# Kernel optimization log

Measured on AMD Instinct MI355X. Metric: run time of the kernel, lower is better.

Reference implementation:

```python
import jax, jax.numpy as jnp
import numpy as np

EMB = 512
HEADS = 8
HEAD_DIM = EMB // HEADS
GN_EPS = 1e-6
THETA_SCALE = 10000.0


def _multiply_by_i(x):
    # interleave: out[..., 2i] = -x[..., 2i+1], out[..., 2i+1] = x[..., 2i]
    return jnp.stack((-x[..., 1::2], x[..., ::2]), axis=-1).reshape(x.shape)


def _theta_shift(x, sin, cos):
    return x * cos + _multiply_by_i(x) * sin


def setup_inputs() -> dict:
    key = jax.random.key(0)
    ks = jax.random.split(key, 13)
    B, N, E = 2, 2048, EMB

    def xavier(k, out_dim, in_dim):
        std = (2.0 / (out_dim + in_dim)) ** 0.5
        return std * jax.random.normal(k, (out_dim, in_dim), dtype=jnp.float32)

    return {
        "query": jax.random.normal(ks[0], (B, N, E), dtype=jnp.float32),
        "k": jax.random.normal(ks[1], (B, N, E), dtype=jnp.float32),
        "v": jax.random.normal(ks[2], (B, N, E), dtype=jnp.float32),
        "Wq": xavier(ks[3], E, E), "bq": jnp.zeros((E,), jnp.float32),
        "Wk": xavier(ks[4], E, E), "bk": jnp.zeros((E,), jnp.float32),
        "Wv": xavier(ks[5], E, E), "bv": jnp.zeros((E,), jnp.float32),
        "Wg": xavier(ks[6], E, E), "bg": jnp.zeros((E,), jnp.float32),
        "Wo": xavier(ks[7], E, E), "bo": jnp.zeros((E,), jnp.float32),
    }


def reference(query, k, v, Wq, bq, Wk, bk, Wv, bv, Wg, bg, Wo, bo):
    B, N, E = query.shape
    H, D = HEADS, E // HEADS

    def proj(x, W, b):  # torch Linear: x @ W.T + b, then split heads -> [b h n d]
        return (x @ W.T + b).reshape(B, N, H, D).transpose(0, 2, 1, 3)

    q = proj(query, Wq, bq)
    kk = proj(k, Wk, bk)
    vv = proj(v, Wv, bv)

    # rotary-style theta shift; thetas repeated pairwise [t0,t0,t1,t1,...]
    thetas = jnp.repeat(1.0 / THETA_SCALE ** jnp.linspace(0.0, 1.0, D // 2), 2)
    angles = jnp.arange(N, dtype=jnp.float32)[:, None] * thetas[None, :]  # [n d]
    sin = jnp.sin(angles)[None, None]
    cos = jnp.cos(angles)[None, None]
    q = _theta_shift(q, sin, cos)
    kk = _theta_shift(kk, sin, cos)

    # decay-masked retention (softmax-free)
    gammas = 1.0 - jnp.exp(jnp.linspace(np.log(1 / 32), np.log(1 / 512), H)).astype(jnp.float32)
    pos = jnp.arange(N)
    dist = jnp.abs(pos[:, None] - pos[None, :]).astype(jnp.float32)
    causal = pos[:, None] >= pos[None, :]
    decay_mask = jnp.where(causal[None], gammas[:, None, None] ** dist[None], 0.0)  # [h n s]

    kk = kk / (D ** 0.5)
    sim = jnp.einsum('bhnd,bhsd->bhns', q, kk) * decay_mask[None]  # [b h n n]
    ret = jnp.einsum('bhns,bhsd->bhnd', sim, vv)

    # GroupNorm(groups=H, channels=H, affine=False) over (b n) samples -> per-(b,h,n) norm over d
    mean = ret.mean(axis=-1, keepdims=True)
    var = ret.var(axis=-1, keepdims=True)
    ret = (ret - mean) / jnp.sqrt(var + GN_EPS)

    ret = ret.transpose(0, 2, 1, 3).reshape(B, N, E)
    gate = jax.nn.silu(query @ Wg.T + bg)
    out = (ret * gate) @ Wo.T + bo
    return out
```

## Files before the change

### kernel.cpp

```cpp
#include <hip/hip_runtime.h>
#include <math.h>

typedef float f32x4 __attribute__((ext_vector_type(4)));
typedef short s16x8 __attribute__((ext_vector_type(8)));
typedef short s16x4 __attribute__((ext_vector_type(4)));
typedef unsigned u32x4 __attribute__((ext_vector_type(4)));

__device__ __forceinline__ short f2bf(float f) {
    unsigned u = __builtin_bit_cast(unsigned, f);
    unsigned r = u + 0x7FFFu + ((u >> 16) & 1u);
    return (short)(r >> 16);
}
__device__ __forceinline__ float bf2f(short h) {
    return __builtin_bit_cast(float, ((unsigned)(unsigned short)h) << 16);
}
__device__ __forceinline__ unsigned pack2(short a, short b) {
    return (unsigned)(unsigned short)a | ((unsigned)(unsigned short)b << 16);
}
__device__ __forceinline__ unsigned cvtpk(float a, float b) {
    unsigned r;
    asm("v_cvt_pk_bf16_f32 %0, %1, %2" : "=v"(r) : "v"(a), "v"(b));
    return r;
}

__device__ __forceinline__ void split16v(const float* __restrict__ p,
                                         short* __restrict__ h,
                                         short* __restrict__ l) {
    f32x4 a0 = *(const f32x4*)(p);
    f32x4 a1 = *(const f32x4*)(p + 4);
    f32x4 a2 = *(const f32x4*)(p + 8);
    f32x4 a3 = *(const f32x4*)(p + 12);
    #pragma unroll
    for (int i = 0; i < 4; ++i) {
        short t0;
        t0 = f2bf(a0[i]); h[i]      = t0; l[i]      = f2bf(a0[i] - bf2f(t0));
        t0 = f2bf(a1[i]); h[4 + i]  = t0; l[4 + i]  = f2bf(a1[i] - bf2f(t0));
        t0 = f2bf(a2[i]); h[8 + i]  = t0; l[8 + i]  = f2bf(a2[i] - bf2f(t0));
        t0 = f2bf(a3[i]); h[12 + i] = t0; l[12 + i] = f2bf(a3[i] - bf2f(t0));
    }
}

__device__ __forceinline__ void gload16(const void* g, void* l) {
    __builtin_amdgcn_global_load_lds(
        (const __attribute__((address_space(1))) unsigned int*)g,
        (__attribute__((address_space(3))) unsigned int*)l,
        16, 0, 0);
}

__device__ __forceinline__ void decay_params(int h, int n0, float& l2g, int& stLo) {
    float lg0 = logf(1.0f / 32.0f), lg1 = logf(1.0f / 512.0f);
    float om = expf(lg0 + (float)h * (lg1 - lg0) * (1.0f / 7.0f));
    l2g = log2f(1.0f - om);
    int Dcut = (int)(11.5129255f / om) + 64;
    stLo = (n0 - Dcut) >> 6;
    if (stLo < 0) stLo = 0;
}

__global__ __launch_bounds__(256) void presplit_kernel(
    const float* __restrict__ W0, const float* __restrict__ W1,
    const float* __restrict__ W2, const float* __restrict__ W3,
    const float* __restrict__ W4,
    short* __restrict__ Wsp, float2* __restrict__ SC)
{
    const int blk = blockIdx.x;
    const int t = threadIdx.x;
    short hbuf[16], lbuf[16];
    if (blk < 256) {
        const int w = blk >> 6, bi = blk & 63;
        const float* src = (w == 0) ? W0 : (w == 1) ? W1 : (w == 2) ? W2 : W3;
        const int idx = (bi * 256 + t) * 16;
        const int row = idx >> 9, k0 = idx & 511;
        const int ntile = row >> 7, r = row & 127;
        const int kstep = k0 >> 5, kk0 = k0 & 31;
        const int s = (r & 3) << 4;
        split16v(src + idx, hbuf, lbuf);
        short* hp = Wsp + (long)w * 524288 + (ntile * 16 + kstep) * 8192 + r * 32;
        short* lp = hp + 4096;
        const int oA = ((2 * kk0) ^ s) >> 1;
        const int oB = ((2 * kk0 + 16) ^ s) >> 1;
        *(s16x8*)(hp + oA) = *(s16x8*)(hbuf);
        *(s16x8*)(hp + oB) = *(s16x8*)(hbuf + 8);
        *(s16x8*)(lp + oA) = *(s16x8*)(lbuf);
        *(s16x8*)(lp + oB) = *(s16x8*)(lbuf + 8);
    } else if (blk < 320) {
        const int bi = blk - 256;
        const int idx = (bi * 256 + t) * 16;
        short* hi = Wsp + (long)4 * 524288;
        short* lo = hi + 262144;
        split16v(W4 + idx, hbuf, lbuf);
        *(s16x8*)(hi + idx)     = *(s16x8*)(hbuf);
        *(s16x8*)(hi + idx + 8) = *(s16x8*)(hbuf + 8);
        *(s16x8*)(lo + idx)     = *(s16x8*)(lbuf);
        *(s16x8*)(lo + idx + 8) = *(s16x8*)(lbuf + 8);
    } else {
        const int gid = (blk - 320) * 256 + t;
        const int pos = gid >> 5, pp = gid & 31;
        const float theta = powf(10000.0f, -(float)pp * (1.0f / 31.0f));
        const float ang = (float)pos * theta;
        SC[gid] = make_float2(cosf(ang), sinf(ang));
    }
}

__global__ __launch_bounds__(512, 4) void projqkvg_kernel(
    const float* __restrict__ X0, const float* __restrict__ X1,
    const float* __restrict__ X2, const short* __restrict__ Wsp,
    const float* __restrict__ bq, const float* __restrict__ bk,
    const float* __restrict__ bv, const float* __restrict__ bg,
    const float2* __restrict__ SC,
    short* __restrict__ Qh, short* __restrict__ Ql,
    short* __restrict__ Kh, short* __restrict__ Vth,
    float* __restrict__ G)
{
    __shared__ __align__(16) short SB[36864];

    const int fid = blockIdx.x + 4 * (blockIdx.y + 64 * blockIdx.z);
    const int mtile = fid & 63;
    const int rr = fid >> 6;
    const int mode = rr & 3;
    const int ntile = rr >> 2;
    const int m0 = mtile * 64, n0 = ntile * 128;

    const int xi = (mode == 1) ? 1 : (mode == 2) ? 2 : 0;
    const float* Xf = (xi == 0) ? X0 : (xi == 1) ? X1 : X2;
    const float* bias = (mode == 0) ? bq : (mode == 1) ? bk
                       : (mode == 2) ? bv : bg;

    const int t = threadIdx.x, lane = t & 63, wv = t >> 6;
    const int wm = wv >> 1, wn = wv & 1;
    const int quad = lane >> 4, l15 = lane & 15;

    const short* Wblk = Wsp + (long)mode * 524288 + (long)ntile * 16 * 8192;

    const int c0 = wv * 3;
    const char* gs[3];
    int gstp[3];
    #pragma unroll
    for (int i = 0; i < 3; ++i) {
        const int c = c0 + i;
        if (c < 8) {
            const int u = c * 64 + lane;
            const int row = u >> 3, ucol = u & 7;
            gs[i] = (const char*)(Xf + (long)(m0 + row) * 512)
                    + ((ucol ^ (row & 7)) << 4);
            gstp[i] = 128;
        } else {
            gs[i] = (const char*)(Wblk + (c - 8) * 512 + lane * 8);
            gstp[i] = 16384;
        }
    }

    auto STAGE = [&](int stg, int ks) {
        char* dstb = (char*)SB + stg * 24576 + c0 * 1024;
        #pragma unroll
        for (int i = 0; i < 3; ++i)
            gload16(gs[i] + (long)ks * gstp[i], dstb + i * 1024);
    };

    int aoff;
    {
        const int row = wm * 16 + l15;
        aoff = row * 128 + ((quad * 32) ^ ((row & 7) << 4));
    }
    const int sxw = (l15 & 3) << 4;
    int boff[4];
    #pragma unroll
    for (int s2 = 0; s2 < 4; ++s2)
        boff[s2] = 8192 + (wn * 64 + s2 * 16 + l15) * 64 + ((quad * 16) ^ sxw);

    f32x4 acc[4];
    #pragma unroll
    for (int j = 0; j < 4; ++j)
        acc[j] = (f32x4){0.f, 0.f, 0.f, 0.f};

    STAGE(0, 0);
    STAGE(1, 1);
    asm volatile("s_waitcnt vmcnt(3)" ::: "memory");
    __builtin_amdgcn_s_barrier();

    int cur = 0;
    for (int ks = 0; ks < 16; ++ks) {
        if (ks < 14) {
            int fill = cur + 2; if (fill >= 3) fill -= 3;
            STAGE(fill, ks + 2);
        }
        __builtin_amdgcn_sched_barrier(0);

        const char* stg = (const char*)SB + cur * 24576;
        s16x8 ah, al, bh[4], bl[4];
        {
            f32x4 x0 = *(const f32x4*)(stg + aoff);
            f32x4 x1 = *(const f32x4*)(stg + (aoff ^ 16));
            u32x4 hv, lv;
            #pragma unroll
            for (int j = 0; j < 2; ++j) {
                float a0 = x0[2 * j], b0 = x0[2 * j + 1];
                float a1 = x1[2 * j], b1 = x1[2 * j + 1];
                unsigned h0 = cvtpk(a0, b0);
                unsigned h1 = cvtpk(a1, b1);
                hv[j]     = h0;
                hv[2 + j] = h1;
                float fa0 = __builtin_bit_cast(float, h0 << 16);
                float fb0 = __builtin_bit_cast(float, h0 & 0xFFFF0000u);
                float fa1 = __builtin_bit_cast(float, h1 << 16);
                float fb1 = __builtin_bit_cast(float, h1 & 0xFFFF0000u);
                lv[j]     = cvtpk(a0 - fa0, b0 - fb0);
                lv[2 + j] = cvtpk(a1 - fa1, b1 - fb1);
            }
            ah = __builtin_bit_cast(s16x8, hv);
            al = __builtin_bit_cast(s16x8, lv);
        }
        #pragma unroll
        for (int s2 = 0; s2 < 4; ++s2) {
            bh[s2] = *(const s16x8*)(stg + boff[s2]);
            bl[s2] = *(const s16x8*)(stg + 8192 + boff[s2]);
        }
        __builtin_amdgcn_s_setprio(1);
        #pragma unroll
        for (int j = 0; j < 4; ++j) {
            acc[j] = __builtin_amdgcn_mfma_f32_16x16x32_bf16(ah, bh[j], acc[j], 0, 0, 0);
            acc[j] = __builtin_amdgcn_mfma_f32_16x16x32_bf16(al, bh[j], acc[j], 0, 0, 0);
            acc[j] = __builtin_amdgcn_mfma_f32_16x16x32_bf16(ah, bl[j], acc[j], 0, 0, 0);
        }
        __builtin_amdgcn_s_setprio(0);

        if (ks < 14)       asm volatile("s_waitcnt vmcnt(3)" ::: "memory");
        else if (ks == 14) asm volatile("s_waitcnt vmcnt(0)" ::: "memory");
        __builtin_amdgcn_sched_barrier(0);
        __builtin_amdgcn_s_barrier();

        cur += 1; if (cur >= 3) cur -= 3;
    }

    __syncthreads();

    const int bb = m0 >> 11, posb = m0 & 2047;
    const int head = (n0 >> 6) + wn;

    if (mode == 0) {
        short* Thi = SB + wv * 2304;
        short* Tlo = Thi + 1152;
        #pragma unroll
        for (int ns = 0; ns < 4; ++ns) {
            const int col = n0 + wn * 64 + ns * 16 + l15;
            const float bvv = bias[col];
            const int pp = (ns * 16 + l15) >> 1;
            #pragma unroll
            for (int r = 0; r < 4; ++r) {
                const int m = m0 + wm * 16 + quad * 4 + r;
                const int pos = m & 2047;
                float x = acc[ns][r] + bvv;
                float prt = __shfl_xor(x, 1);
                float2 sc = SC[pos * 32 + pp];
                float y0 = x * sc.x - prt * sc.y;
                float y1 = prt * sc.x + x * sc.y;
                if (!(l15 & 1)) {
                    short h0 = f2bf(y0), h1 = f2bf(y1);
                    short l0 = f2bf(y0 - bf2f(h0)), l1 = f2bf(y1 - bf2f(h1));
                    const int o = (quad * 4 + r) * 72 + ns * 16 + l15;
                    *(unsigned*)&Thi[o] = pack2(h0, h1);
                    *(unsigned*)&Tlo[o] = pack2(l0, l1);
                }
            }
        }
        #pragma unroll
        for (int p2 = 0; p2 < 2; ++p2) {
            const int row = p2 * 8 + (lane >> 3);
            const int ch = (lane & 7) * 8;
            s16x8 vh = *(const s16x8*)&Thi[row * 72 + ch];
            s16x8 vl = *(const s16x8*)&Tlo[row * 72 + ch];
            const long o = ((long)(bb * 8 + head) * 2048 + posb + wm * 16 + row) * 64 + ch;
            *(s16x8*)(Qh + o) = vh;
            *(s16x8*)(Ql + o) = vl;
        }
    } else if (mode == 1) {
        short* Thi = SB + wv * 1152;
        #pragma unroll
        for (int ns = 0; ns < 4; ++ns) {
            const int col = n0 + wn * 64 + ns * 16 + l15;
            const float bvv = bias[col];
            const int pp = (ns * 16 + l15) >> 1;
            #pragma unroll
            for (int r = 0; r < 4; ++r) {
                const int m = m0 + wm * 16 + quad * 4 + r;
                const int pos = m & 2047;
                float x = acc[ns][r] + bvv;
                float prt = __shfl_xor(x, 1);
                float2 sc = SC[pos * 32 + pp];
                float y0 = (x * sc.x - prt * sc.y) * 0.125f;
                float y1 = (prt * sc.x + x * sc.y) * 0.125f;
                if (!(l15 & 1)) {
                    const int o = (quad * 4 + r) * 72 + ns * 16 + l15;
                    *(unsigned*)&Thi[o] = pack2(f2bf(y0), f2bf(y1));
                }
            }
        }
        #pragma unroll
        for (int p2 = 0; p2 < 2; ++p2) {
            const int row = p2 * 8 + (lane >> 3);
            const int ch = (lane & 7) * 8;
            s16x8 vh = *(const s16x8*)&Thi[row * 72 + ch];
            const long o = ((long)(bb * 8 + head) * 2048 + posb + wm * 16 + row) * 64 + ch;
            *(s16x8*)(Kh + o) = vh;
        }
    } else if (mode == 2) {
        short* T2 = SB;
        #pragma unroll
        for (int ns = 0; ns < 4; ++ns) {
            const int col = n0 + wn * 64 + ns * 16 + l15;
            const float bvv = bias[col];
            s16x4 pk;
            #pragma unroll
            for (int r = 0; r < 4; ++r)
                pk[r] = f2bf(acc[ns][r] + bvv);
            *(s16x4*)&T2[(wn * 64 + ns * 16 + l15) * 72
                         + wm * 16 + quad * 4] = pk;
        }
        __syncthreads();
        #pragma unroll
        for (int pass = 0; pass < 2; ++pass) {
            const int row = pass * 64 + (t >> 3);
            const int ch = (t & 7) * 8;
            s16x8 v = *(const s16x8*)&T2[row * 72 + ch];
            const int hd = (n0 >> 6) + (row >> 6);
            const int d = row & 63;
            const long o = ((long)(bb * 8 + hd) * 64 + d) * 2048 + posb + ch;
            *(s16x8*)(Vth + o) = v;
        }
    } else {
        #pragma unroll
        for (int ns = 0; ns < 4; ++ns) {
            const int col = n0 + wn * 64 + ns * 16 + l15;
            const float bvv = bias[col];
            #pragma unroll
            for (int r = 0; r < 4; ++r) {
                const int m = m0 + wm * 16 + quad * 4 + r;
                float x = acc[ns][r] + bvv;
                G[(long)m * 512 + col] = x / (1.0f + expf(-x));
            }
        }
    }
}

__global__ __launch_bounds__(256) void attn_chunk_kernel(
    const short* __restrict__ Qh_g, const short* __restrict__ Ql_g,
    const short* __restrict__ Kh_g, const short* __restrict__ Vth_g,
    const float* __restrict__ G, short* __restrict__ RGh,
    float* __restrict__ Racc)
{
    __shared__ __align__(16) short KhS[2][4608], VhS[2][4608];
    __shared__ __align__(16) short PhS[4352];

    const int fid = blockIdx.x;
    const int bh = fid & 15;
    const int rest = fid >> 4;
    const int qt = rest & 31;
    const int c  = rest >> 5;
    const int h = bh & 7, b = bh >> 3;
    const int n0 = qt * 64;

    float l2g;
    int stLo;
    decay_params(h, n0, l2g, stLo);
    const int ntiles = qt - stLo + 1;
    const int st0 = stLo + c * 16;
    if (st0 > qt) return;
    const int stHi = min(st0 + 15, qt);

    const int t = threadIdx.x, lane = t & 63, wv = t >> 6;
    const int quad = lane >> 4, l15 = lane & 15;
    const long base = (long)bh * 2048 * 64;

    float gneg[16];
    #pragma unroll
    for (int i = 0; i < 16; ++i)
        gneg[i] = exp2f(-(float)((i >> 2) * 16 + (i & 3)) * l2g);

    const int srow = t >> 2;
    const int scol = (t & 3) * 16;
    const int n = n0 + wv * 16 + l15;

    s16x8 qh[2], ql[2];
    {
        const short* qp  = Qh_g + base + (long)(n0 + wv * 16 + l15) * 64 + quad * 8;
        const short* qp2 = Ql_g + base + (long)(n0 + wv * 16 + l15) * 64 + quad * 8;
        qh[0] = *(const s16x8*)qp;
        qh[1] = *(const s16x8*)(qp + 32);
        ql[0] = *(const s16x8*)qp2;
        ql[1] = *(const s16x8*)(qp2 + 32);
    }

    f32x4 racc[4];
    #pragma unroll
    for (int i = 0; i < 4; ++i) racc[i] = (f32x4){0.f, 0.f, 0.f, 0.f};

    s16x8 pk0, pk1, pv0, pv1;
    {
        const long ko = base + (long)(st0 * 64 + srow) * 64 + scol;
        pk0 = *(const s16x8*)(Kh_g + ko);
        pk1 = *(const s16x8*)(Kh_g + ko + 8);
        const long vo = base + (long)srow * 2048 + st0 * 64 + scol;
        pv0 = *(const s16x8*)(Vth_g + vo);
        pv1 = *(const s16x8*)(Vth_g + vo + 8);
    }
    *(s16x8*)&KhS[0][srow * 72 + scol]     = pk0;
    *(s16x8*)&KhS[0][srow * 72 + scol + 8] = pk1;
    *(s16x8*)&VhS[0][srow * 72 + scol]     = pv0;
    *(s16x8*)&VhS[0][srow * 72 + scol + 8] = pv1;
    __syncthreads();

    int cur = 0;
    for (int st = st0; st <= stHi; ++st, cur ^= 1) {
        if (st < stHi) {
            const long ko = base + (long)((st + 1) * 64 + srow) * 64 + scol;
            pk0 = *(const s16x8*)(Kh_g + ko);
            pk1 = *(const s16x8*)(Kh_g + ko + 8);
            const long vo = base + (long)srow * 2048 + (st + 1) * 64 + scol;
            pv0 = *(const s16x8*)(Vth_g + vo);
            pv1 = *(const s16x8*)(Vth_g + vo + 8);
        }

        const short* khs = KhS[cur];
        const short* vhs = VhS[cur];
        const int s0 = st * 64;
        const float t0 = exp2f((float)(n - s0 - quad * 4) * l2g);

        #pragma unroll
        for (int sub = 0; sub < 4; ++sub) {
            const int ro = (sub * 16 + l15) * 72 + quad * 8;
            s16x8 kh0 = *(const s16x8*)&khs[ro];
            s16x8 kh1 = *(const s16x8*)&khs[ro + 32];
            f32x4 sacc = (f32x4){0.f, 0.f, 0.f, 0.f};
            __builtin_amdgcn_s_setprio(1);
            sacc = __builtin_amdgcn_mfma_f32_16x16x32_bf16(kh0, qh[0], sacc, 0, 0, 0);
            sacc = __builtin_amdgcn_mfma_f32_16x16x32_bf16(kh1, qh[1], sacc, 0, 0, 0);
            sacc = __builtin_amdgcn_mfma_f32_16x16x32_bf16(kh0, ql[0], sacc, 0, 0, 0);
            sacc = __builtin_amdgcn_mfma_f32_16x16x32_bf16(kh1, ql[1], sacc, 0, 0, 0);
            __builtin_amdgcn_s_setprio(0);

            const int sb = s0 + sub * 16 + quad * 4;
            s16x4 pkh;
            #pragma unroll
            for (int r = 0; r < 4; ++r) {
                const int s = sb + r;
                const float wgt = (n >= s) ? t0 * gneg[sub * 4 + r] : 0.0f;
                pkh[r] = f2bf(sacc[r] * wgt);
            }
            *(s16x4*)&PhS[(wv * 16 + l15) * 68 + sub * 16 + quad * 4] = pkh;
        }

        const int pro = (wv * 16 + l15) * 68 + quad * 8;
        s16x8 ph0 = *(const s16x8*)&PhS[pro];
        s16x8 ph1 = *(const s16x8*)&PhS[pro + 32];
        __builtin_amdgcn_s_setprio(1);
        #pragma unroll
        for (int ds = 0; ds < 4; ++ds) {
            const int ro = (ds * 16 + l15) * 72 + quad * 8;
            s16x8 vh0 = *(const s16x8*)&vhs[ro];
            s16x8 vh1 = *(const s16x8*)&vhs[ro + 32];
            racc[ds] = __builtin_amdgcn_mfma_f32_16x16x32_bf16(ph0, vh0, racc[ds], 0, 0, 0);
            racc[ds] = __builtin_amdgcn_mfma_f32_16x16x32_bf16(ph1, vh1, racc[ds], 0, 0, 0);
        }
        __builtin_amdgcn_s_setprio(0);

        if (st < stHi) {
            short* kd = KhS[cur ^ 1];
            short* vd = VhS[cur ^ 1];
            *(s16x8*)&kd[srow * 72 + scol]     = pk0;
            *(s16x8*)&kd[srow * 72 + scol + 8] = pk1;
            *(s16x8*)&vd[srow * 72 + scol]     = pv0;
            *(s16x8*)&vd[srow * 72 + scol + 8] = pv1;
        }
        __syncthreads();
    }

    if (c == 0 && ntiles <= 16) {
        float mean[4], rstd[4];
        #pragma unroll
        for (int r = 0; r < 4; ++r) {
            float s = racc[0][r] + racc[1][r] + racc[2][r] + racc[3][r];
            s += __shfl_xor(s, 1); s += __shfl_xor(s, 2);
            s += __shfl_xor(s, 4); s += __shfl_xor(s, 8);
            mean[r] = s * (1.0f / 64.0f);
            float vs = 0.f;
            #pragma unroll
            for (int ds = 0; ds < 4; ++ds) {
                float d = racc[ds][r] - mean[r];
                vs += d * d;
            }
            vs += __shfl_xor(vs, 1); vs += __shfl_xor(vs, 2);
            vs += __shfl_xor(vs, 4); vs += __shfl_xor(vs, 8);
            rstd[r] = rsqrtf(vs * (1.0f / 64.0f) + 1e-6f);
        }
        short* rgH = (short*)KhS + wv * 1152;
        #pragma unroll
        for (int ds = 0; ds < 4; ++ds) {
            #pragma unroll
            for (int r = 0; r < 4; ++r) {
                const int nn = n0 + wv * 16 + quad * 4 + r;
                const int d = ds * 16 + l15;
                const long gi = ((long)(b * 2048 + nn)) * 512 + h * 64 + d;
                float rg = (racc[ds][r] - mean[r]) * rstd[r] * G[gi];
                float prt = __shfl_xor(rg, 1);
                if (!(l15 & 1)) {
                    const int o = (quad * 4 + r) * 72 + ds * 16 + l15;
                    *(unsigned*)&rgH[o] = pack2(f2bf(rg), f2bf(prt));
                }
            }
        }
        #pragma unroll
        for (int p2 = 0; p2 < 2; ++p2) {
            const int row = p2 * 8 + (lane >> 3);
            const int ch = (lane & 7) * 8;
            s16x8 vh = *(const s16x8*)&rgH[row * 72 + ch];
            const int nn = n0 + wv * 16 + row;
            const long o = ((long)(b * 2048 + nn)) * 512 + h * 64 + ch;
            *(s16x8*)(RGh + o) = vh;
        }
        return;
    }

    float* dst = Racc + (long)((bh * 32 + qt) * 2 + c) * 4096;
    #pragma unroll
    for (int ds = 0; ds < 4; ++ds)
        #pragma unroll
        for (int r = 0; r < 4; ++r)
            dst[(wv * 16 + quad * 4 + r) * 64 + ds * 16 + l15] = racc[ds][r];
}

__global__ __launch_bounds__(256) void attn_finish_kernel(
    const float* __restrict__ Racc, const float* __restrict__ G,
    short* __restrict__ RGh)
{
    __shared__ __align__(16) short rgS[4608];

    const int fid = blockIdx.x;
    const int bh = fid & 15;
    const int qt = fid >> 4;
    const int h = bh & 7, b = bh >> 3;
    const int n0 = qt * 64;

    float l2g;
    int stLo;
    decay_params(h, n0, l2g, stLo);
    const int ntiles = qt - stLo + 1;
    if (ntiles <= 16) return;

    const int t = threadIdx.x, lane = t & 63, wv = t >> 6;
    const int quad = lane >> 4, l15 = lane & 15;

    const float* s0 = Racc + (long)((bh * 32 + qt) * 2) * 4096;
    f32x4 racc[4];
    #pragma unroll
    for (int ds = 0; ds < 4; ++ds)
        #pragma unroll
        for (int r = 0; r < 4; ++r) {
            const int o = (wv * 16 + quad * 4 + r) * 64 + ds * 16 + l15;
            racc[ds][r] = s0[o] + s0[4096 + o];
        }

    float mean[4], rstd[4];
    #pragma unroll
    for (int r = 0; r < 4; ++r) {
        float s = racc[0][r] + racc[1][r] + racc[2][r] + racc[3][r];
        s += __shfl_xor(s, 1); s += __shfl_xor(s, 2);
        s += __shfl_xor(s, 4); s += __shfl_xor(s, 8);
        mean[r] = s * (1.0f / 64.0f);
        float vs = 0.f;
        #pragma unroll
        for (int ds = 0; ds < 4; ++ds) {
            float d = racc[ds][r] - mean[r];
            vs += d * d;
        }
        vs += __shfl_xor(vs, 1); vs += __shfl_xor(vs, 2);
        vs += __shfl_xor(vs, 4); vs += __shfl_xor(vs, 8);
        rstd[r] = rsqrtf(vs * (1.0f / 64.0f) + 1e-6f);
    }

    short* rgH = rgS + wv * 1152;
    #pragma unroll
    for (int ds = 0; ds < 4; ++ds) {
        #pragma unroll
        for (int r = 0; r < 4; ++r) {
            const int nn = n0 + wv * 16 + quad * 4 + r;
            const int d = ds * 16 + l15;
            const long gi = ((long)(b * 2048 + nn)) * 512 + h * 64 + d;
            float rg = (racc[ds][r] - mean[r]) * rstd[r] * G[gi];
            float prt = __shfl_xor(rg, 1);
            if (!(l15 & 1)) {
                const int o = (quad * 4 + r) * 72 + ds * 16 + l15;
                *(unsigned*)&rgH[o] = pack2(f2bf(rg), f2bf(prt));
            }
        }
    }
    __syncthreads();
    #pragma unroll
    for (int p2 = 0; p2 < 2; ++p2) {
        const int row = p2 * 8 + (lane >> 3);
        const int ch = (lane & 7) * 8;
        s16x8 vh = *(const s16x8*)&rgS[(wv * 1152 + row * 72 + ch)];
        const int nn = n0 + wv * 16 + row;
        const long o = ((long)(b * 2048 + nn)) * 512 + h * 64 + ch;
        *(s16x8*)(RGh + o) = vh;
    }
}

__global__ __launch_bounds__(256) void projo_kernel(
    const short* __restrict__ RGh, const short* __restrict__ Woh_g,
    const float* __restrict__ bo, float* __restrict__ out)
{
    __shared__ __align__(16) char PB[46080];

    const short* Wol_g = Woh_g + 262144;
    const int t = threadIdx.x, lane = t & 63, wv = t >> 6;
    const int wm = wv >> 1, wn = wv & 1;
    const int quad = lane >> 4, l15 = lane & 15;
    const int m0 = blockIdx.y * 32, n0 = blockIdx.x * 128;

    f32x4 acc[4];
    #pragma unroll
    for (int j = 0; j < 4; ++j) acc[j] = (f32x4){0.f, 0.f, 0.f, 0.f};

    const int xrow = t >> 3, xcol = (t & 7) * 4;
    const int wrow = t >> 1, wcol = (t & 1) * 16;
    const long xbase = (long)(m0 + xrow) * 512 + xcol;
    const long wbase = (long)(n0 + wrow) * 512 + wcol;

    s16x4 px;
    s16x8 pw0, pw1, pw2, pw3;
    px  = *(const s16x4*)(RGh + xbase);
    pw0 = *(const s16x8*)(Woh_g + wbase);
    pw1 = *(const s16x8*)(Woh_g + wbase + 8);
    pw2 = *(const s16x8*)(Wol_g + wbase);
    pw3 = *(const s16x8*)(Wol_g + wbase + 8);

    {
        short* XhS = (short*)PB;
        short* WhS = XhS + 1280;
        short* WlS = XhS + 6400;
        *(s16x4*)&XhS[xrow * 40 + xcol]     = px;
        *(s16x8*)&WhS[wrow * 40 + wcol]     = pw0;
        *(s16x8*)&WhS[wrow * 40 + wcol + 8] = pw1;
        *(s16x8*)&WlS[wrow * 40 + wcol]     = pw2;
        *(s16x8*)&WlS[wrow * 40 + wcol + 8] = pw3;
    }
    __syncthreads();

    for (int k0 = 0; k0 < 512; k0 += 32) {
        const int cur = (k0 >> 5) & 1;
        const bool more = (k0 + 32 < 512);
        if (more) {
            const long xo = xbase + k0 + 32;
            const long wo = wbase + k0 + 32;
            px  = *(const s16x4*)(RGh + xo);
            pw0 = *(const s16x8*)(Woh_g + wo);
            pw1 = *(const s16x8*)(Woh_g + wo + 8);
            pw2 = *(const s16x8*)(Wol_g + wo);
            pw3 = *(const s16x8*)(Wol_g + wo + 8);
        }

        const short* XhS = (const short*)(PB + cur * 23040);
        const short* WhS = XhS + 1280;
        const short* WlS = XhS + 6400;
        s16x8 ah, bh[4], bl[4];
        {
            const int ro = (wm * 16 + l15) * 40 + quad * 8;
            ah = *(const s16x8*)&XhS[ro];
        }
        #pragma unroll
        for (int s = 0; s < 4; ++s) {
            const int ro = (wn * 64 + s * 16 + l15) * 40 + quad * 8;
            bh[s] = *(const s16x8*)&WhS[ro];
            bl[s] = *(const s16x8*)&WlS[ro];
        }
        #pragma unroll
        for (int j = 0; j < 4; ++j) {
            acc[j] = __builtin_amdgcn_mfma_f32_16x16x32_bf16(ah, bh[j], acc[j], 0, 0, 0);
            acc[j] = __builtin_amdgcn_mfma_f32_16x16x32_bf16(ah, bl[j], acc[j], 0, 0, 0);
        }

        if (more) {
            short* XhD = (short*)(PB + (cur ^ 1) * 23040);
            short* WhD = XhD + 1280;
            short* WlD = XhD + 6400;
            *(s16x4*)&XhD[xrow * 40 + xcol]     = px;
            *(s16x8*)&WhD[wrow * 40 + wcol]     = pw0;
            *(s16x8*)&WhD[wrow * 40 + wcol + 8] = pw1;
            *(s16x8*)&WlD[wrow * 40 + wcol]     = pw2;
            *(s16x8*)&WlD[wrow * 40 + wcol + 8] = pw3;
        }
        __syncthreads();
    }

    float* T = (float*)PB + wv * 1152;
    #pragma unroll
    for (int ns = 0; ns < 4; ++ns) {
        const int col = n0 + wn * 64 + ns * 16 + l15;
        const float bvv = bo[col];
        #pragma unroll
        for (int r = 0; r < 4; ++r)
            T[(quad * 4 + r) * 72 + ns * 16 + l15] = acc[ns][r] + bvv;
    }
    #pragma unroll
    for (int it = 0; it < 2; ++it) {
        const int row = it * 8 + (lane >> 3);
        const int ch = (lane & 7) * 8;
        f32x4 a = *(const f32x4*)&T[row * 72 + ch];
        f32x4 c = *(const f32x4*)&T[row * 72 + ch + 4];
        const long o = (long)(m0 + wm * 16 + row) * 512 + n0 + wn * 64 + ch;
        *(f32x4*)(out + o) = a;
        *(f32x4*)(out + o + 4) = c;
    }
}

extern "C" void kernel_launch(void* const* d_in, const int* in_sizes, int n_in,
                              void* d_out, int out_size, void* d_ws, size_t ws_size,
                              hipStream_t stream) {
    const float* query = (const float*)d_in[0];
    const float* kin   = (const float*)d_in[1];
    const float* vin   = (const float*)d_in[2];
    const float* Wq = (const float*)d_in[3];
    const float* bq = (const float*)d_in[4];
    const float* Wk = (const float*)d_in[5];
    const float* bk = (const float*)d_in[6];
    const float* Wv = (const float*)d_in[7];
    const float* bv = (const float*)d_in[8];
    const float* Wg = (const float*)d_in[9];
    const float* bg = (const float*)d_in[10];
    const float* Wo = (const float*)d_in[11];
    const float* bo = (const float*)d_in[12];

    short* S = (short*)d_ws;
    const long NE = 2097152;
    short* WSp = S;
    short* Xsp = S + 2621440;
    short* Qh  = Xsp + 12582912;
    short* Ql  = Qh + NE;
    short* Kh  = Ql + NE;
    short* Vth = Kh + NE;
    float* G   = (float*)(Vth + NE);
    short* RGh = (short*)(G + NE);
    float2* SC = (float2*)(RGh + NE);
    float* Racc = (float*)Xsp;

    presplit_kernel<<<576, 256, 0, stream>>>(
        Wq, Wk, Wv, Wg, Wo, WSp, SC);
    projqkvg_kernel<<<dim3(4, 64, 4), 512, 0, stream>>>(
        query, kin, vin, WSp, bq, bk, bv, bg, SC, Qh, Ql, Kh, Vth, G);
    attn_chunk_kernel<<<1024, 256, 0, stream>>>(
        Qh, Ql, Kh, Vth, G, RGh, Racc);
    attn_finish_kernel<<<512, 256, 0, stream>>>(
        Racc, G, RGh);
    projo_kernel<<<dim3(4, 128), 256, 0, stream>>>(
        RGh, WSp + 4 * 524288, bo, (float*)d_out);
}
```

Measured before the change: 181.5 us.

## Load projection activations directly into registers instead of staging through LDS

The projection kernel no longer stages the fp32 activation tile through shared memory. Each lane now loads its own A fragment straight from global memory into registers, prefetched two k-steps ahead, and only the split-bf16 weights stay in the 3-stage LDS pipeline. This cuts LDS use per block, so launch bounds rise to 6 blocks per SM for more occupancy. The trade-off is uncoalesced, redundant global reads of X across waves that share rows, plus more live registers and a vmcnt accounting that must stay correct.

```diff
diff --git a/kernel.cpp b/kernel.cpp
--- a/kernel.cpp
+++ b/kernel.cpp
@@ -101,7 +101,7 @@
     }
 }
 
-__global__ __launch_bounds__(512, 4) void projqkvg_kernel(
+__global__ __launch_bounds__(512, 6) void projqkvg_kernel(
     const float* __restrict__ X0, const float* __restrict__ X1,
     const float* __restrict__ X2, const short* __restrict__ Wsp,
     const float* __restrict__ bq, const float* __restrict__ bk,
@@ -111,7 +111,7 @@
     short* __restrict__ Kh, short* __restrict__ Vth,
     float* __restrict__ G)
 {
-    __shared__ __align__(16) short SB[36864];
+    __shared__ __align__(16) short SB[24576];
 
     const int fid = blockIdx.x + 4 * (blockIdx.y + 64 * blockIdx.z);
     const int mtile = fid & 63;
@@ -131,70 +131,60 @@
 
     const short* Wblk = Wsp + (long)mode * 524288 + (long)ntile * 16 * 8192;
 
-    const int c0 = wv * 3;
-    const char* gs[3];
-    int gstp[3];
-    #pragma unroll
-    for (int i = 0; i < 3; ++i) {
-        const int c = c0 + i;
-        if (c < 8) {
-            const int u = c * 64 + lane;
-            const int row = u >> 3, ucol = u & 7;
-            gs[i] = (const char*)(Xf + (long)(m0 + row) * 512)
-                    + ((ucol ^ (row & 7)) << 4);
-            gstp[i] = 128;
-        } else {
-            gs[i] = (const char*)(Wblk + (c - 8) * 512 + lane * 8);
-            gstp[i] = 16384;
-        }
-    }
+    const int c0 = wv * 2;
+    const char* gs[2];
+    #pragma unroll
+    for (int i = 0; i < 2; ++i)
+        gs[i] = (const char*)(Wblk + (c0 + i) * 512 + lane * 8);
 
     auto STAGE = [&](int stg, int ks) {
-        char* dstb = (char*)SB + stg * 24576 + c0 * 1024;
-        #pragma unroll
-        for (int i = 0; i < 3; ++i)
-            gload16(gs[i] + (long)ks * gstp[i], dstb + i * 1024);
+        char* dstb = (char*)SB + stg * 16384 + c0 * 1024;
+        #pragma unroll
+        for (int i = 0; i < 2; ++i)
+            gload16(gs[i] + (long)ks * 16384, dstb + i * 1024);
     };
 
-    int aoff;
-    {
-        const int row = wm * 16 + l15;
-        aoff = row * 128 + ((quad * 32) ^ ((row & 7) << 4));
-    }
+    const float* xp = Xf + (long)(m0 + wm * 16 + l15) * 512 + quad * 8;
+
     const int sxw = (l15 & 3) << 4;
     int boff[4];
     #pragma unroll
     for (int s2 = 0; s2 < 4; ++s2)
-        boff[s2] = 8192 + (wn * 64 + s2 * 16 + l15) * 64 + ((quad * 16) ^ sxw);
+        boff[s2] = (wn * 64 + s2 * 16 + l15) * 64 + ((quad * 16) ^ sxw);
 
     f32x4 acc[4];
     #pragma unroll
     for (int j = 0; j < 4; ++j)
         acc[j] = (f32x4){0.f, 0.f, 0.f, 0.f};
 
+    f32x4 x0c = *(const f32x4*)(xp);
+    f32x4 x1c = *(const f32x4*)(xp + 4);
+    f32x4 x0n = *(const f32x4*)(xp + 32);
+    f32x4 x1n = *(const f32x4*)(xp + 36);
     STAGE(0, 0);
     STAGE(1, 1);
-    asm volatile("s_waitcnt vmcnt(3)" ::: "memory");
+    asm volatile("s_waitcnt vmcnt(2)" ::: "memory");
     __builtin_amdgcn_s_barrier();
 
     int cur = 0;
     for (int ks = 0; ks < 16; ++ks) {
+        f32x4 x0f = x0c, x1f = x1c;
         if (ks < 14) {
+            x0f = *(const f32x4*)(xp + (ks + 2) * 32);
+            x1f = *(const f32x4*)(xp + (ks + 2) * 32 + 4);
             int fill = cur + 2; if (fill >= 3) fill -= 3;
             STAGE(fill, ks + 2);
         }
         __builtin_amdgcn_sched_barrier(0);
 
-        const char* stg = (const char*)SB + cur * 24576;
+        const char* stg = (const char*)SB + cur * 16384;
         s16x8 ah, al, bh[4], bl[4];
         {
-            f32x4 x0 = *(const f32x4*)(stg + aoff);
-            f32x4 x1 = *(const f32x4*)(stg + (aoff ^ 16));
             u32x4 hv, lv;
             #pragma unroll
             for (int j = 0; j < 2; ++j) {
-                float a0 = x0[2 * j], b0 = x0[2 * j + 1];
-                float a1 = x1[2 * j], b1 = x1[2 * j + 1];
+                float a0 = x0c[2 * j], b0 = x0c[2 * j + 1];
+                float a1 = x1c[2 * j], b1 = x1c[2 * j + 1];
                 unsigned h0 = cvtpk(a0, b0);
                 unsigned h1 = cvtpk(a1, b1);
                 hv[j]     = h0;
@@ -223,11 +213,12 @@
         }
         __builtin_amdgcn_s_setprio(0);
 
-        if (ks < 14)       asm volatile("s_waitcnt vmcnt(3)" ::: "memory");
+        if (ks < 14)       asm volatile("s_waitcnt vmcnt(4)" ::: "memory");
         else if (ks == 14) asm volatile("s_waitcnt vmcnt(0)" ::: "memory");
         __builtin_amdgcn_sched_barrier(0);
         __builtin_amdgcn_s_barrier();
 
+        x0c = x0n; x1c = x1n; x0n = x0f; x1n = x1f;
         cur += 1; if (cur >= 3) cur -= 3;
     }
 
```

New measurement: 199.3 us. 1.1x slower.
